# Optimization experiments

Hardware: AMD Instinct MI355X
Metric: run time of the kernel (lower is better)

The kernel has to match this reference:

```python
import jax, jax.numpy as jnp
import numpy as np

NU, NT, E, H, NL, NVOC, OUT, HID2 = 100000, 400000, 400000, 128, 3, 10000, 2, 64
EPS = 1e-5


def setup_inputs() -> dict:
    key = jax.random.key(0)
    ks = jax.random.split(key, 20)
    s = 1.0 / np.sqrt(H).astype(np.float32)
    inp = {
        "x_user": jax.random.randint(ks[0], (NU,), 0, NVOC),
        "x_txn": jax.random.randint(ks[1], (NT,), 0, NVOC),
        "ei0_src": jax.random.randint(ks[2], (E,), 0, NU),
        "ei0_dst": jax.random.randint(ks[3], (E,), 0, NT),
        "ei1_src": jax.random.randint(ks[4], (E,), 0, NT),
        "ei1_dst": jax.random.randint(ks[5], (E,), 0, NU),
        "emb_user": jax.random.normal(ks[6], (NVOC, H), jnp.float32),
        "emb_txn": jax.random.normal(ks[7], (NVOC, H), jnp.float32),
        "Wl": jax.random.normal(ks[8], (NL, 2, H, H), jnp.float32) * s,
        "bl": jax.random.normal(ks[9], (NL, 2, H), jnp.float32) * 0.01,
        "Wr": jax.random.normal(ks[10], (NL, 2, H, H), jnp.float32) * s,
        "bn_gamma": jax.random.uniform(ks[11], (NL, 2, H), jnp.float32, 0.5, 1.5),
        "bn_beta": jax.random.normal(ks[12], (NL, 2, H), jnp.float32) * 0.01,
        "bn_mean": jax.random.normal(ks[13], (NL, 2, H), jnp.float32) * 0.01,
        "bn_var": jax.random.uniform(ks[14], (NL, 2, H), jnp.float32, 0.5, 1.5),
        "W1": jax.random.normal(ks[15], (H, HID2), jnp.float32) * s,
        "b1": jax.random.normal(ks[16], (HID2,), jnp.float32) * 0.01,
        "W2": jax.random.normal(ks[17], (HID2, OUT), jnp.float32) * (1.0 / np.sqrt(HID2).astype(np.float32)),
        "b2": jax.random.normal(ks[18], (OUT,), jnp.float32) * 0.01,
    }
    return inp


def _seg_mean(src_feat, src_idx, dst_idx, num_dst):
    # gather per-edge src features, mean-reduce per dst node (SAGEConv aggr='mean')
    msg = src_feat[src_idx]                                        # [E, H]
    tot = jax.ops.segment_sum(msg, dst_idx, num_segments=num_dst)  # [Ndst, H]
    cnt = jax.ops.segment_sum(jnp.ones((dst_idx.shape[0], 1), src_feat.dtype),
                              dst_idx, num_segments=num_dst)
    return tot / jnp.maximum(cnt, 1.0)


def _bn_relu(x, g, b, m, v):
    return jax.nn.relu((x - m) * jax.lax.rsqrt(v + EPS) * g + b)


def reference(x_user, x_txn, ei0_src, ei0_dst, ei1_src, ei1_dst,
              emb_user, emb_txn, Wl, bl, Wr,
              bn_gamma, bn_beta, bn_mean, bn_var, W1, b1, W2, b2):
    h_u = emb_user[x_user]   # [NU, H]
    h_t = emb_txn[x_txn]     # [NT, H]
    for i in range(NL):
        # edge type 0: user -> transaction; edge type 1: transaction -> user
        agg_t = _seg_mean(h_u, ei0_src, ei0_dst, h_t.shape[0])
        agg_u = _seg_mean(h_t, ei1_src, ei1_dst, h_u.shape[0])
        new_t = agg_t @ Wl[i, 0] + bl[i, 0] + h_t @ Wr[i, 0]
        new_u = agg_u @ Wl[i, 1] + bl[i, 1] + h_u @ Wr[i, 1]
        h_u = _bn_relu(new_u, bn_gamma[i, 0], bn_beta[i, 0], bn_mean[i, 0], bn_var[i, 0])
        h_t = _bn_relu(new_t, bn_gamma[i, 1], bn_beta[i, 1], bn_mean[i, 1], bn_var[i, 1])
    h = jnp.concatenate([h_u, h_t], axis=0)            # [NU+NT, H]
    out = jax.nn.relu(h @ W1 + b1) @ W2 + b2           # [NU+NT, OUT]
    return out
```

## Files before the change

### kernel.cpp

```cpp
#include <hip/hip_runtime.h>


#define NUv   100000
#define NTv   400000
#define Ev    400000
#define Hv    128
#define NLv   3
#define HID2v 64
#define EPSv  1e-5f

typedef _Float16 h16;
typedef __attribute__((ext_vector_type(8))) _Float16 f16x8;
typedef __attribute__((ext_vector_type(4))) float    f32x4;

#define WS_NEED (280u * 1024u * 1024u)
__device__ __attribute__((aligned(256))) static unsigned char g_ws[WS_NEED];

__device__ __forceinline__ int imin(int a, int b) { return a < b ? a : b; }
__device__ __forceinline__ int swz(int n, int kbyte) {
  return n * 256 + (kbyte ^ ((n & 7) << 4));
}
__device__ __forceinline__ int swzB(int n, int kbyte) {
  return n * 512 + (kbyte ^ ((n & 7) << 4));
}

__global__ __launch_bounds__(256) void k_count(const int* __restrict__ d0,
                                               const int* __restrict__ d1,
                                               int* __restrict__ c0,
                                               int* __restrict__ c1, int e) {
  int t = blockIdx.x * 256 + threadIdx.x;
  if (t < e) {
    atomicAdd(c0 + d0[t], 1);
    atomicAdd(c1 + d1[t], 1);
  }
}

__global__ __launch_bounds__(256) void k_blocksum2(const int* __restrict__ c0,
                                                   int n0, int g0,
                                                   const int* __restrict__ c1,
                                                   int n1,
                                                   int* __restrict__ bs0,
                                                   int* __restrict__ bs1) {
  __shared__ int red[256];
  int second = blockIdx.x >= g0 ? 1 : 0;
  const int* cnt = second ? c1 : c0;
  int n = second ? n1 : n0;
  int* bs = second ? bs1 : bs0;
  int bid = blockIdx.x - (second ? g0 : 0);
  int base = bid * 2048 + threadIdx.x * 8;
  int s = 0;
#pragma unroll
  for (int j = 0; j < 8; j++) {
    int p = base + j;
    if (p < n) s += cnt[p];
  }
  red[threadIdx.x] = s;
  __syncthreads();
  for (int st = 128; st > 0; st >>= 1) {
    if (threadIdx.x < st) red[threadIdx.x] += red[threadIdx.x + st];
    __syncthreads();
  }
  if (threadIdx.x == 0) bs[bid] = red[0];
}

__global__ __launch_bounds__(256) void k_scansmall2(int* __restrict__ bs0, int g0,
                                                    int* __restrict__ bs1, int g1) {
  __shared__ int lds[256];
  int* bs = blockIdx.x ? bs1 : bs0;
  int g = blockIdx.x ? g1 : g0;
  int t = threadIdx.x;
  int v = (t < g) ? bs[t] : 0;
  lds[t] = v;
  __syncthreads();
  for (int st = 1; st < 256; st <<= 1) {
    int x = (t >= st) ? lds[t - st] : 0;
    __syncthreads();
    lds[t] += x;
    __syncthreads();
  }
  if (t < g) bs[t] = lds[t] - v;
}

__global__ __launch_bounds__(256) void k_scanfinal2(const int* __restrict__ c0,
                                                    int n0, int g0,
                                                    const int* __restrict__ bs0,
                                                    int* __restrict__ off0,
                                                    int* __restrict__ cur0,
                                                    const int* __restrict__ c1,
                                                    int n1,
                                                    const int* __restrict__ bs1,
                                                    int* __restrict__ off1,
                                                    int* __restrict__ cur1) {
  __shared__ int lds[256];
  int second = blockIdx.x >= g0 ? 1 : 0;
  const int* cnt = second ? c1 : c0;
  const int* bs = second ? bs1 : bs0;
  int* off = second ? off1 : off0;
  int* cur = second ? cur1 : cur0;
  int n = second ? n1 : n0;
  int bid = blockIdx.x - (second ? g0 : 0);
  int t = threadIdx.x;
  int base = bid * 2048 + t * 8;
  int v[8], pre[8];
  int tsum = 0;
#pragma unroll
  for (int j = 0; j < 8; j++) {
    int p = base + j;
    v[j] = (p < n) ? cnt[p] : 0;
    pre[j] = tsum;
    tsum += v[j];
  }
  lds[t] = tsum;
  __syncthreads();
  for (int st = 1; st < 256; st <<= 1) {
    int x = (t >= st) ? lds[t - st] : 0;
    __syncthreads();
    lds[t] += x;
    __syncthreads();
  }
  int texcl = lds[t] - tsum;
  int boff = bs[bid];
#pragma unroll
  for (int j = 0; j < 8; j++) {
    int p = base + j;
    if (p < n) {
      int o = boff + texcl + pre[j];
      off[p] = o;
      cur[p] = o;
      if (p == n - 1) off[n] = o + v[j];
    }
  }
}

__global__ __launch_bounds__(256) void k_fill(const int* __restrict__ s0,
                                              const int* __restrict__ d0,
                                              const int* __restrict__ s1,
                                              const int* __restrict__ d1,
                                              int* __restrict__ cur0,
                                              int* __restrict__ cur1,
                                              int* __restrict__ ss0,
                                              int* __restrict__ ss1, int e) {
  int t = blockIdx.x * 256 + threadIdx.x;
  if (t < e) {
    int p = atomicAdd(cur0 + d0[t], 1);
    ss0[p] = s0[t];
    int q = atomicAdd(cur1 + d1[t], 1);
    ss1[q] = s1[t];
  }
}

__global__ __launch_bounds__(256) void k_wtbn(const float* __restrict__ Wl,
                                              const float* __restrict__ Wr,
                                              const float* __restrict__ W1,
                                              const float* __restrict__ g,
                                              const float* __restrict__ b,
                                              const float* __restrict__ m,
                                              const float* __restrict__ v,
                                              h16* __restrict__ WlT,
                                              h16* __restrict__ WrT,
                                              h16* __restrict__ W1T,
                                              float* __restrict__ sc,
                                              float* __restrict__ sh) {
  int t = blockIdx.x * 256 + threadIdx.x;
  const int NW = NLv * 2 * Hv * Hv;
  const int NW1 = NW + HID2v * Hv;
  if (t < NW) {
    int mat = t / (Hv * Hv);
    int n = (t / Hv) % Hv;
    int k = t % Hv;
    WlT[t] = (h16)Wl[(size_t)mat * Hv * Hv + (size_t)k * Hv + n];
    WrT[t] = (h16)Wr[(size_t)mat * Hv * Hv + (size_t)k * Hv + n];
  } else if (t < NW1) {
    int u = t - NW;
    int n = u / Hv;
    int k = u % Hv;
    W1T[u] = (h16)W1[(size_t)k * HID2v + n];
  } else if (t < NW1 + NLv * 2 * Hv) {
    int u = t - NW1;
    float inv = rsqrtf(v[u] + EPSv);
    float s = g[u] * inv;
    sc[u] = s;
    sh[u] = b[u] - m[u] * s;
  }
}

__global__ __launch_bounds__(256) void k_embed(const int* __restrict__ xu,
                                               const int* __restrict__ xt,
                                               const float* __restrict__ eu,
                                               const float* __restrict__ et,
                                               h16* __restrict__ hu,
                                               h16* __restrict__ ht) {
  int t = blockIdx.x * 256 + threadIdx.x;
  int row = t >> 4;
  int c = (t & 15) * 8;
  if (row >= NUv + NTv) return;
  const float* src;
  h16* dst;
  if (row < NUv) {
    src = eu + (size_t)xu[row] * Hv;
    dst = hu + (size_t)row * Hv;
  } else {
    int r2 = row - NUv;
    src = et + (size_t)xt[r2] * Hv;
    dst = ht + (size_t)r2 * Hv;
  }
  float4 v0 = *(const float4*)(src + c);
  float4 v1 = *(const float4*)(src + c + 4);
  f16x8 o;
  o[0] = (h16)v0.x; o[1] = (h16)v0.y; o[2] = (h16)v0.z; o[3] = (h16)v0.w;
  o[4] = (h16)v1.x; o[5] = (h16)v1.y; o[6] = (h16)v1.z; o[7] = (h16)v1.w;
  *(f16x8*)(dst + c) = o;
}

__global__ __launch_bounds__(512, 4) void k_fused2(
    const h16* __restrict__ SRC0, const h16* __restrict__ DEN0,
    const int* __restrict__ offA, const int* __restrict__ ssA,
    const h16* __restrict__ BTl0, const h16* __restrict__ BTr0,
    const float* __restrict__ blp0, const float* __restrict__ scp0,
    const float* __restrict__ shp0, h16* __restrict__ C0, int M0,
    const h16* __restrict__ SRC1, const h16* __restrict__ DEN1,
    const int* __restrict__ offB, const int* __restrict__ ssB,
    const h16* __restrict__ BTl1, const h16* __restrict__ BTr1,
    const float* __restrict__ blp1, const float* __restrict__ scp1,
    const float* __restrict__ shp1, h16* __restrict__ C1, int M1) {
  __shared__ __align__(16) unsigned char sB[128 * 512];
  __shared__ __align__(16) unsigned char sA[64 * 256];

  int t = threadIdx.x;
  int l = t & 63, lm = l & 15, lk = l >> 4;
  int w = t >> 6, rg = w >> 1, cg = w & 1;

  int nT0 = (M0 + 63) / 64;
  int nT1 = (M1 + 63) / 64;
  int nTot = nT0 + nT1;
  int curDir = -1;

  for (int gidx = blockIdx.x; gidx < nTot; gidx += gridDim.x) {
    int dir = (gidx < nT0) ? 0 : 1;
    const h16* SRC = dir ? SRC1 : SRC0;
    const h16* DENSE = dir ? DEN1 : DEN0;
    const int* off = dir ? offB : offA;
    const int* ss = dir ? ssB : ssA;
    const float* blp = dir ? blp1 : blp0;
    const float* scp = dir ? scp1 : scp0;
    const float* shp = dir ? shp1 : shp0;
    h16* C = dir ? C1 : C0;
    int M = dir ? M1 : M0;
    int base = (dir ? gidx - nT0 : gidx) * 64;

    if (dir != curDir) {
      const h16* BTr = dir ? BTr1 : BTr0;
      const h16* BTl = dir ? BTl1 : BTl0;
      int n = t >> 2;
      int kb = (t & 3) * 64;
      const h16* sr = BTr + t * 32;
      f16x8 r0 = *(const f16x8*)(sr + 0);
      f16x8 r1 = *(const f16x8*)(sr + 8);
      f16x8 r2 = *(const f16x8*)(sr + 16);
      f16x8 r3 = *(const f16x8*)(sr + 24);
      const h16* sl = BTl + t * 32;
      f16x8 l0 = *(const f16x8*)(sl + 0);
      f16x8 l1 = *(const f16x8*)(sl + 8);
      f16x8 l2 = *(const f16x8*)(sl + 16);
      f16x8 l3 = *(const f16x8*)(sl + 24);
      *(f16x8*)(sB + swzB(n, kb + 0)) = r0;
      *(f16x8*)(sB + swzB(n, kb + 16)) = r1;
      *(f16x8*)(sB + swzB(n, kb + 32)) = r2;
      *(f16x8*)(sB + swzB(n, kb + 48)) = r3;
      *(f16x8*)(sB + swzB(n, 256 + kb + 0)) = l0;
      *(f16x8*)(sB + swzB(n, 256 + kb + 16)) = l1;
      *(f16x8*)(sB + swzB(n, 256 + kb + 32)) = l2;
      *(f16x8*)(sB + swzB(n, 256 + kb + 48)) = l3;
      __syncthreads();
      curDir = dir;
    }

    int ar = imin(base + rg * 16 + lm, M - 1);
    const h16* arow = DENSE + (size_t)ar * Hv;
    f16x8 ad0 = *(const f16x8*)(arow + 0 * 32 + lk * 8);
    f16x8 ad1 = *(const f16x8*)(arow + 1 * 32 + lk * 8);
    f16x8 ad2 = *(const f16x8*)(arow + 2 * 32 + lk * 8);
    f16x8 ad3 = *(const f16x8*)(arow + 3 * 32 + lk * 8);

    {
      int r = t >> 3;
      int cs = (t & 7) * 16;
      float facc[16];
#pragma unroll
      for (int j = 0; j < 16; j++) facc[j] = 0.f;
      int row = base + r;
      if (row < M) {
        int e0 = off[row], e1 = off[row + 1];
        for (int e = e0; e < e1; e += 2) {
          int i0 = ss[e];
          bool v1 = (e + 1) < e1;
          int i1 = v1 ? ss[e + 1] : i0;
          const f16x8* p0 = (const f16x8*)(SRC + (size_t)i0 * Hv + cs);
          const f16x8* p1 = (const f16x8*)(SRC + (size_t)i1 * Hv + cs);
          f16x8 x0 = p0[0], x1 = p0[1];
          f16x8 y0 = p1[0], y1 = p1[1];
          float m1 = v1 ? 1.f : 0.f;
#pragma unroll
          for (int j = 0; j < 8; j++) {
            facc[j] += (float)x0[j];
            facc[8 + j] += (float)x1[j];
            facc[j] = fmaf((float)y0[j], m1, facc[j]);
            facc[8 + j] = fmaf((float)y1[j], m1, facc[8 + j]);
          }
        }
        int deg = e1 - e0;
        float inv = 1.f / (float)(deg > 1 ? deg : 1);
#pragma unroll
        for (int j = 0; j < 16; j++) facc[j] *= inv;
      }
#pragma unroll
      for (int q = 0; q < 2; q++) {
        f16x8 ov;
#pragma unroll
        for (int j = 0; j < 8; j++) ov[j] = (h16)facc[q * 8 + j];
        *(f16x8*)(sA + swz(r, cs * 2 + q * 16)) = ov;
      }
    }
    __syncthreads();

    f32x4 acc[4];
#pragma unroll
    for (int j = 0; j < 4; j++) acc[j] = (f32x4){0.f, 0.f, 0.f, 0.f};
    {
      f16x8 ads[4] = {ad0, ad1, ad2, ad3};
#pragma unroll
      for (int s = 0; s < 4; s++) {
#pragma unroll
        for (int j = 0; j < 4; j++) {
          int n = (cg * 4 + j) * 16 + lm;
          f16x8 b = *(const f16x8*)(sB + swzB(n, s * 64 + lk * 16));
          acc[j] = __builtin_amdgcn_mfma_f32_16x16x32_f16(ads[s], b, acc[j], 0, 0, 0);
        }
      }
#pragma unroll
      for (int s = 0; s < 4; s++) {
        f16x8 a = *(const f16x8*)(sA + swz(rg * 16 + lm, s * 64 + lk * 16));
#pragma unroll
        for (int j = 0; j < 4; j++) {
          int n = (cg * 4 + j) * 16 + lm;
          f16x8 b = *(const f16x8*)(sB + swzB(n, 256 + s * 64 + lk * 16));
          acc[j] = __builtin_amdgcn_mfma_f32_16x16x32_f16(a, b, acc[j], 0, 0, 0);
        }
      }
    }

#pragma unroll
    for (int j = 0; j < 4; j++) {
      int col = (cg * 4 + j) * 16 + lm;
      float blv = blp[col], scv = scp[col], shv = shp[col];
#pragma unroll
      for (int r_ = 0; r_ < 4; r_++) {
        int row = base + rg * 16 + lk * 4 + r_;
        if (row < M) {
          float x = fmaf(acc[j][r_] + blv, scv, shv);
          C[(size_t)row * Hv + col] = (h16)fmaxf(x, 0.f);
        }
      }
    }
    __syncthreads();
  }
}

__global__ __launch_bounds__(512, 4) void k_mlp(const h16* __restrict__ HU,
                                                const h16* __restrict__ HT,
                                                const h16* __restrict__ W1T,
                                                const float* __restrict__ b1,
                                                const float* __restrict__ W2,
                                                const float* __restrict__ b2,
                                                float* __restrict__ out, int Mtot) {
  __shared__ float y[128][65];
  __shared__ __align__(16) unsigned char sW[64 * 256];
  int t = threadIdx.x;
  int w = t >> 6, l = t & 63;
  int lm = l & 15, lk = l >> 4;

  {
    const h16* src = W1T + t * 16;
    f16x8 w0 = *(const f16x8*)(src + 0);
    f16x8 w1 = *(const f16x8*)(src + 8);
    int n = (t * 16) >> 7;
    int kb = ((t * 16) & 127) * 2;
    *(f16x8*)(sW + swz(n, kb + 0)) = w0;
    *(f16x8*)(sW + swz(n, kb + 16)) = w1;
  }

  int rowBase = blockIdx.x * 128 + w * 16;
  int ar = imin(rowBase + lm, Mtot - 1);
  const h16* arow =
      (ar < NUv) ? (HU + (size_t)ar * Hv) : (HT + (size_t)(ar - NUv) * Hv);
  f16x8 a0 = *(const f16x8*)(arow + 0 * 32 + lk * 8);
  f16x8 a1 = *(const f16x8*)(arow + 1 * 32 + lk * 8);
  f16x8 a2 = *(const f16x8*)(arow + 2 * 32 + lk * 8);
  f16x8 a3 = *(const f16x8*)(arow + 3 * 32 + lk * 8);
  __syncthreads();

  f32x4 acc[4];
#pragma unroll
  for (int nf = 0; nf < 4; nf++) acc[nf] = (f32x4){0.f, 0.f, 0.f, 0.f};
  {
    f16x8 as[4] = {a0, a1, a2, a3};
#pragma unroll
    for (int s = 0; s < 4; s++) {
#pragma unroll
      for (int nf = 0; nf < 4; nf++) {
        f16x8 b = *(const f16x8*)(sW + swz(nf * 16 + lm, s * 64 + lk * 16));
        acc[nf] = __builtin_amdgcn_mfma_f32_16x16x32_f16(as[s], b, acc[nf], 0, 0, 0);
      }
    }
  }
#pragma unroll
  for (int nf = 0; nf < 4; nf++) {
    int col = nf * 16 + lm;
    float b1v = b1[col];
#pragma unroll
    for (int r = 0; r < 4; r++) {
      int rloc = w * 16 + lk * 4 + r;
      y[rloc][col] = fmaxf(acc[nf][r] + b1v, 0.f);
    }
  }
  __syncthreads();
  if (t < 256) {
    int rloc = t >> 1, o = t & 1;
    int row = blockIdx.x * 128 + rloc;
    if (row < Mtot) {
      float sum = b2[o];
#pragma unroll
      for (int k = 0; k < HID2v; k++) sum += y[rloc][k] * W2[k * 2 + o];
      out[(size_t)row * 2 + o] = sum;
    }
  }
}

extern "C" void kernel_launch(void* const* d_in, const int* in_sizes, int n_in,
                              void* d_out, int out_size, void* d_ws, size_t ws_size,
                              hipStream_t stream) {
  (void)in_sizes; (void)n_in; (void)out_size;

  const int* x_user  = (const int*)d_in[0];
  const int* x_txn   = (const int*)d_in[1];
  const int* ei0_src = (const int*)d_in[2];
  const int* ei0_dst = (const int*)d_in[3];
  const int* ei1_src = (const int*)d_in[4];
  const int* ei1_dst = (const int*)d_in[5];
  const float* emb_user = (const float*)d_in[6];
  const float* emb_txn  = (const float*)d_in[7];
  const float* Wl = (const float*)d_in[8];
  const float* bl = (const float*)d_in[9];
  const float* Wr = (const float*)d_in[10];
  const float* bn_g = (const float*)d_in[11];
  const float* bn_b = (const float*)d_in[12];
  const float* bn_m = (const float*)d_in[13];
  const float* bn_v = (const float*)d_in[14];
  const float* W1 = (const float*)d_in[15];
  const float* b1 = (const float*)d_in[16];
  const float* W2 = (const float*)d_in[17];
  const float* b2 = (const float*)d_in[18];
  float* out = (float*)d_out;

  char* wsb;
  if (ws_size >= (size_t)WS_NEED) {
    wsb = (char*)d_ws;
  } else {
    void* sym = nullptr;
    hipGetSymbolAddress(&sym, HIP_SYMBOL(g_ws));
    wsb = (char*)sym;
  }
  size_t o = 0;
  auto alloc = [&](size_t bytes) -> void* {
    o = (o + 255) & ~(size_t)255;
    void* p = wsb + o;
    o += bytes;
    return p;
  };
  h16* hu0  = (h16*)alloc((size_t)NUv * Hv * 2);
  h16* hu1  = (h16*)alloc((size_t)NUv * Hv * 2);
  h16* ht0  = (h16*)alloc((size_t)NTv * Hv * 2);
  h16* ht1  = (h16*)alloc((size_t)NTv * Hv * 2);
  h16* WlT  = (h16*)alloc((size_t)NLv * 2 * Hv * Hv * 2);
  h16* WrT  = (h16*)alloc((size_t)NLv * 2 * Hv * Hv * 2);
  h16* W1T  = (h16*)alloc((size_t)HID2v * Hv * 2);
  float* bnsc = (float*)alloc((size_t)NLv * 2 * Hv * 4);
  float* bnsh = (float*)alloc((size_t)NLv * 2 * Hv * 4);
  int* off0 = (int*)alloc((size_t)(NTv + 1) * 4);
  int* off1 = (int*)alloc((size_t)(NUv + 1) * 4);
  int* cur0 = (int*)alloc((size_t)NTv * 4);
  int* cur1 = (int*)alloc((size_t)NUv * 4);
  int* ss0  = (int*)alloc((size_t)Ev * 4);
  int* ss1  = (int*)alloc((size_t)Ev * 4);
  int* bs0  = (int*)alloc(256 * 4);
  int* bs1  = (int*)alloc(256 * 4);

  const int G_E    = (Ev + 255) / 256;
  const int G_BS0  = (NTv + 2047) / 2048;
  const int G_BS1  = (NUv + 2047) / 2048;
  const int G_EMB  = ((NUv + NTv) * 16 + 255) / 256;
  const int N_WTBN = NLv * 2 * Hv * Hv + HID2v * Hv + NLv * 2 * Hv;
  const int G_WTBN = (N_WTBN + 255) / 256;
  const int G_F    = 512;
  const int G_MLP  = (NUv + NTv + 127) / 128;

  hipMemsetAsync(cur0, 0, (size_t)NTv * 4, stream);
  hipMemsetAsync(cur1, 0, (size_t)NUv * 4, stream);
  k_count<<<G_E, 256, 0, stream>>>(ei0_dst, ei1_dst, cur0, cur1, Ev);
  k_blocksum2<<<G_BS0 + G_BS1, 256, 0, stream>>>(cur0, NTv, G_BS0, cur1, NUv,
                                                 bs0, bs1);
  k_scansmall2<<<2, 256, 0, stream>>>(bs0, G_BS0, bs1, G_BS1);
  k_scanfinal2<<<G_BS0 + G_BS1, 256, 0, stream>>>(cur0, NTv, G_BS0, bs0, off0,
                                                  cur0, cur1, NUv, bs1, off1,
                                                  cur1);
  k_fill<<<G_E, 256, 0, stream>>>(ei0_src, ei0_dst, ei1_src, ei1_dst,
                                  cur0, cur1, ss0, ss1, Ev);

  k_wtbn<<<G_WTBN, 256, 0, stream>>>(Wl, Wr, W1, bn_g, bn_b, bn_m, bn_v,
                                     WlT, WrT, W1T, bnsc, bnsh);

  k_embed<<<G_EMB, 256, 0, stream>>>(x_user, x_txn, emb_user, emb_txn, hu0, ht0);

  h16* hu_cur = hu0; h16* hu_nxt = hu1;
  h16* ht_cur = ht0; h16* ht_nxt = ht1;
  for (int i = 0; i < NLv; i++) {
    const h16* WlT0 = WlT + (size_t)(i * 2 + 0) * Hv * Hv;
    const h16* WlT1 = WlT + (size_t)(i * 2 + 1) * Hv * Hv;
    const h16* WrT0 = WrT + (size_t)(i * 2 + 0) * Hv * Hv;
    const h16* WrT1 = WrT + (size_t)(i * 2 + 1) * Hv * Hv;
    const float* bl0 = bl + (size_t)(i * 2 + 0) * Hv;
    const float* bl1 = bl + (size_t)(i * 2 + 1) * Hv;
    const float* sc0 = bnsc + (size_t)(i * 2 + 0) * Hv;
    const float* sh0 = bnsh + (size_t)(i * 2 + 0) * Hv;
    const float* sc1 = bnsc + (size_t)(i * 2 + 1) * Hv;
    const float* sh1 = bnsh + (size_t)(i * 2 + 1) * Hv;

    k_fused2<<<G_F, 512, 0, stream>>>(
        hu_cur, ht_cur, off0, ss0, WlT0, WrT0, bl0, sc1, sh1, ht_nxt, NTv,
        ht_cur, hu_cur, off1, ss1, WlT1, WrT1, bl1, sc0, sh0, hu_nxt, NUv);
    h16* tmp;
    tmp = ht_cur; ht_cur = ht_nxt; ht_nxt = tmp;
    tmp = hu_cur; hu_cur = hu_nxt; hu_nxt = tmp;
  }

  k_mlp<<<G_MLP, 512, 0, stream>>>(hu_cur, ht_cur, W1T, b1, W2, b2, out,
                                   NUv + NTv);
}
```

Measured before the change: 706.8 us.

## Restructure fused SAGE layer to per-wave 16-row tiles without LDS staging

The combined two-direction kernel becomes a single-direction kernel launched twice per layer. Each wave now owns a 16-row tile: it gathers neighbour features straight into MFMA A-operand registers, dropping the shared-memory A buffer and the per-tile block barriers. The bias is folded into the BN shift and the scale/shift values are hoisted out of the loop. In exchange it adds an extra launch per layer and higher register pressure from 32 float accumulators and 8 MFMA accumulators. Bounds checks are removed, so the code relies on M being a multiple of 16.

```diff
diff --git a/kernel.cpp b/kernel.cpp
--- a/kernel.cpp
+++ b/kernel.cpp
@@ -212,157 +212,128 @@
   *(f16x8*)(dst + c) = o;
 }
 
-__global__ __launch_bounds__(512, 4) void k_fused2(
-    const h16* __restrict__ SRC0, const h16* __restrict__ DEN0,
-    const int* __restrict__ offA, const int* __restrict__ ssA,
-    const h16* __restrict__ BTl0, const h16* __restrict__ BTr0,
-    const float* __restrict__ blp0, const float* __restrict__ scp0,
-    const float* __restrict__ shp0, h16* __restrict__ C0, int M0,
-    const h16* __restrict__ SRC1, const h16* __restrict__ DEN1,
-    const int* __restrict__ offB, const int* __restrict__ ssB,
-    const h16* __restrict__ BTl1, const h16* __restrict__ BTr1,
-    const float* __restrict__ blp1, const float* __restrict__ scp1,
-    const float* __restrict__ shp1, h16* __restrict__ C1, int M1) {
+__global__ __launch_bounds__(512, 4) void k_fused(const h16* __restrict__ SRC,
+                                                  const h16* __restrict__ DENSE,
+                                                  const int* __restrict__ off,
+                                                  const int* __restrict__ ss,
+                                                  const h16* __restrict__ BTl,
+                                                  const h16* __restrict__ BTr,
+                                                  const float* __restrict__ bl,
+                                                  const float* __restrict__ sc,
+                                                  const float* __restrict__ sh,
+                                                  h16* __restrict__ C, int M) {
   __shared__ __align__(16) unsigned char sB[128 * 512];
-  __shared__ __align__(16) unsigned char sA[64 * 256];
 
   int t = threadIdx.x;
   int l = t & 63, lm = l & 15, lk = l >> 4;
-  int w = t >> 6, rg = w >> 1, cg = w & 1;
-
-  int nT0 = (M0 + 63) / 64;
-  int nT1 = (M1 + 63) / 64;
-  int nTot = nT0 + nT1;
-  int curDir = -1;
-
-  for (int gidx = blockIdx.x; gidx < nTot; gidx += gridDim.x) {
-    int dir = (gidx < nT0) ? 0 : 1;
-    const h16* SRC = dir ? SRC1 : SRC0;
-    const h16* DENSE = dir ? DEN1 : DEN0;
-    const int* off = dir ? offB : offA;
-    const int* ss = dir ? ssB : ssA;
-    const float* blp = dir ? blp1 : blp0;
-    const float* scp = dir ? scp1 : scp0;
-    const float* shp = dir ? shp1 : shp0;
-    h16* C = dir ? C1 : C0;
-    int M = dir ? M1 : M0;
-    int base = (dir ? gidx - nT0 : gidx) * 64;
-
-    if (dir != curDir) {
-      const h16* BTr = dir ? BTr1 : BTr0;
-      const h16* BTl = dir ? BTl1 : BTl0;
-      int n = t >> 2;
-      int kb = (t & 3) * 64;
-      const h16* sr = BTr + t * 32;
-      f16x8 r0 = *(const f16x8*)(sr + 0);
-      f16x8 r1 = *(const f16x8*)(sr + 8);
-      f16x8 r2 = *(const f16x8*)(sr + 16);
-      f16x8 r3 = *(const f16x8*)(sr + 24);
-      const h16* sl = BTl + t * 32;
-      f16x8 l0 = *(const f16x8*)(sl + 0);
-      f16x8 l1 = *(const f16x8*)(sl + 8);
-      f16x8 l2 = *(const f16x8*)(sl + 16);
-      f16x8 l3 = *(const f16x8*)(sl + 24);
-      *(f16x8*)(sB + swzB(n, kb + 0)) = r0;
-      *(f16x8*)(sB + swzB(n, kb + 16)) = r1;
-      *(f16x8*)(sB + swzB(n, kb + 32)) = r2;
-      *(f16x8*)(sB + swzB(n, kb + 48)) = r3;
-      *(f16x8*)(sB + swzB(n, 256 + kb + 0)) = l0;
-      *(f16x8*)(sB + swzB(n, 256 + kb + 16)) = l1;
-      *(f16x8*)(sB + swzB(n, 256 + kb + 32)) = l2;
-      *(f16x8*)(sB + swzB(n, 256 + kb + 48)) = l3;
-      __syncthreads();
-      curDir = dir;
-    }
-
-    int ar = imin(base + rg * 16 + lm, M - 1);
-    const h16* arow = DENSE + (size_t)ar * Hv;
-    f16x8 ad0 = *(const f16x8*)(arow + 0 * 32 + lk * 8);
-    f16x8 ad1 = *(const f16x8*)(arow + 1 * 32 + lk * 8);
-    f16x8 ad2 = *(const f16x8*)(arow + 2 * 32 + lk * 8);
-    f16x8 ad3 = *(const f16x8*)(arow + 3 * 32 + lk * 8);
-
+  int w = t >> 6;
+
+  {
+    int n = t >> 2;
+    int kb = (t & 3) * 64;
+    const h16* sr = BTr + t * 32;
+    f16x8 r0 = *(const f16x8*)(sr + 0);
+    f16x8 r1 = *(const f16x8*)(sr + 8);
+    f16x8 r2 = *(const f16x8*)(sr + 16);
+    f16x8 r3 = *(const f16x8*)(sr + 24);
+    const h16* sl = BTl + t * 32;
+    f16x8 l0 = *(const f16x8*)(sl + 0);
+    f16x8 l1 = *(const f16x8*)(sl + 8);
+    f16x8 l2 = *(const f16x8*)(sl + 16);
+    f16x8 l3 = *(const f16x8*)(sl + 24);
+    *(f16x8*)(sB + swzB(n, kb + 0)) = r0;
+    *(f16x8*)(sB + swzB(n, kb + 16)) = r1;
+    *(f16x8*)(sB + swzB(n, kb + 32)) = r2;
+    *(f16x8*)(sB + swzB(n, kb + 48)) = r3;
+    *(f16x8*)(sB + swzB(n, 256 + kb + 0)) = l0;
+    *(f16x8*)(sB + swzB(n, 256 + kb + 16)) = l1;
+    *(f16x8*)(sB + swzB(n, 256 + kb + 32)) = l2;
+    *(f16x8*)(sB + swzB(n, 256 + kb + 48)) = l3;
+  }
+
+  float scv[8], shv[8];
+#pragma unroll
+  for (int j = 0; j < 8; j++) {
+    int col = j * 16 + lm;
+    float s = sc[col];
+    scv[j] = s;
+    shv[j] = fmaf(bl[col], s, sh[col]);
+  }
+  __syncthreads();
+
+  int nWT = M >> 4;
+  for (int wt = blockIdx.x * 8 + w; wt < nWT; wt += gridDim.x * 8) {
+    int base = wt << 4;
+    int rowA = base + lm;
+
+    const h16* arow = DENSE + (size_t)rowA * Hv + lk * 8;
+    f16x8 ad0 = *(const f16x8*)(arow);
+    f16x8 ad1 = *(const f16x8*)(arow + 32);
+    f16x8 ad2 = *(const f16x8*)(arow + 64);
+    f16x8 ad3 = *(const f16x8*)(arow + 96);
+
+    float facc[32];
+#pragma unroll
+    for (int j = 0; j < 32; j++) facc[j] = 0.f;
+    int e0 = off[rowA], e1 = off[rowA + 1];
+    for (int e = e0; e < e1; ++e) {
+      const h16* sp = SRC + (size_t)ss[e] * Hv + lk * 8;
+      f16x8 v0 = *(const f16x8*)(sp);
+      f16x8 v1 = *(const f16x8*)(sp + 32);
+      f16x8 v2 = *(const f16x8*)(sp + 64);
+      f16x8 v3 = *(const f16x8*)(sp + 96);
+#pragma unroll
+      for (int j = 0; j < 8; j++) {
+        facc[j] += (float)v0[j];
+        facc[8 + j] += (float)v1[j];
+        facc[16 + j] += (float)v2[j];
+        facc[24 + j] += (float)v3[j];
+      }
+    }
     {
-      int r = t >> 3;
-      int cs = (t & 7) * 16;
-      float facc[16];
-#pragma unroll
-      for (int j = 0; j < 16; j++) facc[j] = 0.f;
-      int row = base + r;
-      if (row < M) {
-        int e0 = off[row], e1 = off[row + 1];
-        for (int e = e0; e < e1; e += 2) {
-          int i0 = ss[e];
-          bool v1 = (e + 1) < e1;
-          int i1 = v1 ? ss[e + 1] : i0;
-          const f16x8* p0 = (const f16x8*)(SRC + (size_t)i0 * Hv + cs);
-          const f16x8* p1 = (const f16x8*)(SRC + (size_t)i1 * Hv + cs);
-          f16x8 x0 = p0[0], x1 = p0[1];
-          f16x8 y0 = p1[0], y1 = p1[1];
-          float m1 = v1 ? 1.f : 0.f;
-#pragma unroll
-          for (int j = 0; j < 8; j++) {
-            facc[j] += (float)x0[j];
-            facc[8 + j] += (float)x1[j];
-            facc[j] = fmaf((float)y0[j], m1, facc[j]);
-            facc[8 + j] = fmaf((float)y1[j], m1, facc[8 + j]);
-          }
-        }
-        int deg = e1 - e0;
-        float inv = 1.f / (float)(deg > 1 ? deg : 1);
-#pragma unroll
-        for (int j = 0; j < 16; j++) facc[j] *= inv;
-      }
-#pragma unroll
-      for (int q = 0; q < 2; q++) {
-        f16x8 ov;
-#pragma unroll
-        for (int j = 0; j < 8; j++) ov[j] = (h16)facc[q * 8 + j];
-        *(f16x8*)(sA + swz(r, cs * 2 + q * 16)) = ov;
-      }
-    }
-    __syncthreads();
-
-    f32x4 acc[4];
-#pragma unroll
-    for (int j = 0; j < 4; j++) acc[j] = (f32x4){0.f, 0.f, 0.f, 0.f};
+      int deg = e1 - e0;
+      float inv = 1.f / (float)(deg > 1 ? deg : 1);
+#pragma unroll
+      for (int j = 0; j < 32; j++) facc[j] *= inv;
+    }
+    f16x8 aA0, aA1, aA2, aA3;
+#pragma unroll
+    for (int j = 0; j < 8; j++) {
+      aA0[j] = (h16)facc[j];
+      aA1[j] = (h16)facc[8 + j];
+      aA2[j] = (h16)facc[16 + j];
+      aA3[j] = (h16)facc[24 + j];
+    }
+
+    f32x4 acc[8];
+#pragma unroll
+    for (int j = 0; j < 8; j++) acc[j] = (f32x4){0.f, 0.f, 0.f, 0.f};
     {
       f16x8 ads[4] = {ad0, ad1, ad2, ad3};
+      f16x8 aAs[4] = {aA0, aA1, aA2, aA3};
 #pragma unroll
       for (int s = 0; s < 4; s++) {
 #pragma unroll
-        for (int j = 0; j < 4; j++) {
-          int n = (cg * 4 + j) * 16 + lm;
-          f16x8 b = *(const f16x8*)(sB + swzB(n, s * 64 + lk * 16));
-          acc[j] = __builtin_amdgcn_mfma_f32_16x16x32_f16(ads[s], b, acc[j], 0, 0, 0);
+        for (int j = 0; j < 8; j++) {
+          int n = j * 16 + lm;
+          f16x8 br = *(const f16x8*)(sB + swzB(n, s * 64 + lk * 16));
+          acc[j] = __builtin_amdgcn_mfma_f32_16x16x32_f16(ads[s], br, acc[j], 0, 0, 0);
+          f16x8 bw = *(const f16x8*)(sB + swzB(n, 256 + s * 64 + lk * 16));
+          acc[j] = __builtin_amdgcn_mfma_f32_16x16x32_f16(aAs[s], bw, acc[j], 0, 0, 0);
         }
       }
-#pragma unroll
-      for (int s = 0; s < 4; s++) {
-        f16x8 a = *(const f16x8*)(sA + swz(rg * 16 + lm, s * 64 + lk * 16));
-#pragma unroll
-        for (int j = 0; j < 4; j++) {
-          int n = (cg * 4 + j) * 16 + lm;
-          f16x8 b = *(const f16x8*)(sB + swzB(n, 256 + s * 64 + lk * 16));
-          acc[j] = __builtin_amdgcn_mfma_f32_16x16x32_f16(a, b, acc[j], 0, 0, 0);
-        }
+    }
+
+#pragma unroll
+    for (int j = 0; j < 8; j++) {
+      int col = j * 16 + lm;
+#pragma unroll
+      for (int r_ = 0; r_ < 4; r_++) {
+        int row = base + lk * 4 + r_;
+        float x = fmaf(acc[j][r_], scv[j], shv[j]);
+        C[(size_t)row * Hv + col] = (h16)fmaxf(x, 0.f);
       }
     }
-
-#pragma unroll
-    for (int j = 0; j < 4; j++) {
-      int col = (cg * 4 + j) * 16 + lm;
-      float blv = blp[col], scv = scp[col], shv = shp[col];
-#pragma unroll
-      for (int r_ = 0; r_ < 4; r_++) {
-        int row = base + rg * 16 + lk * 4 + r_;
-        if (row < M) {
-          float x = fmaf(acc[j][r_] + blv, scv, shv);
-          C[(size_t)row * Hv + col] = (h16)fmaxf(x, 0.f);
-        }
-      }
-    }
-    __syncthreads();
   }
 }
 
@@ -535,9 +506,10 @@
     const float* sc1 = bnsc + (size_t)(i * 2 + 1) * Hv;
     const float* sh1 = bnsh + (size_t)(i * 2 + 1) * Hv;
 
-    k_fused2<<<G_F, 512, 0, stream>>>(
-        hu_cur, ht_cur, off0, ss0, WlT0, WrT0, bl0, sc1, sh1, ht_nxt, NTv,
-        ht_cur, hu_cur, off1, ss1, WlT1, WrT1, bl1, sc0, sh0, hu_nxt, NUv);
+    k_fused<<<G_F, 512, 0, stream>>>(hu_cur, ht_cur, off0, ss0, WlT0, WrT0,
+                                     bl0, sc1, sh1, ht_nxt, NTv);
+    k_fused<<<G_F, 512, 0, stream>>>(ht_cur, hu_cur, off1, ss1, WlT1, WrT1,
+                                     bl1, sc0, sh0, hu_nxt, NUv);
     h16* tmp;
     tmp = ht_cur; ht_cur = ht_nxt; ht_nxt = tmp;
     tmp = hu_cur; hu_cur = hu_nxt; hu_nxt = tmp;
```

Result: slower. 2.002 ms (+183.2%).

## Sort destination rows by in-degree and split fused layer into per-direction launches

Applied to the files above, without the earlier changes.

Adds a degree-histogram counting sort that builds a permutation of destination rows grouped by in-degree. The fused aggregate+GEMM kernel then processes rows in that order, so rows within a tile have similar edge counts and per-thread gather loops are more balanced. The single two-direction kernel is split into two launches, each loading its weights once up front, and bias is folded into the BN shift. The cost is three extra preprocessing kernels, an indirection through perm on dense loads and output stores, scattered row writes, and a launch boundary between the two directions.

```diff
diff --git a/kernel.cpp b/kernel.cpp
--- a/kernel.cpp
+++ b/kernel.cpp
@@ -146,6 +146,79 @@
     ss0[p] = s0[t];
     int q = atomicAdd(cur1 + d1[t], 1);
     ss1[q] = s1[t];
+  }
+}
+
+__global__ __launch_bounds__(256) void k_deghist2(const int* __restrict__ off0,
+                                                  int n0, int g0,
+                                                  const int* __restrict__ off1,
+                                                  int n1,
+                                                  int* __restrict__ h0,
+                                                  int* __restrict__ h1) {
+  __shared__ int lh[32];
+  int t = threadIdx.x;
+  if (t < 32) lh[t] = 0;
+  __syncthreads();
+  int second = blockIdx.x >= g0 ? 1 : 0;
+  const int* off = second ? off1 : off0;
+  int n = second ? n1 : n0;
+  int* h = second ? h1 : h0;
+  int r = (blockIdx.x - (second ? g0 : 0)) * 256 + t;
+  if (r < n) {
+    int d = off[r + 1] - off[r];
+    if (d > 31) d = 31;
+    atomicAdd(&lh[d], 1);
+  }
+  __syncthreads();
+  if (t < 32 && lh[t]) atomicAdd(&h[t], lh[t]);
+}
+
+__global__ __launch_bounds__(64) void k_degscan2(int* __restrict__ h0,
+                                                 int* __restrict__ h1) {
+  int* h = blockIdx.x ? h1 : h0;
+  if (threadIdx.x == 0) {
+    int s = 0;
+    for (int i = 0; i < 32; i++) {
+      int v = h[i];
+      h[i] = s;
+      s += v;
+    }
+  }
+}
+
+__global__ __launch_bounds__(256) void k_degscatter2(const int* __restrict__ off0,
+                                                     int n0, int g0,
+                                                     const int* __restrict__ off1,
+                                                     int n1,
+                                                     int* __restrict__ cur0,
+                                                     int* __restrict__ cur1,
+                                                     int* __restrict__ p0,
+                                                     int* __restrict__ p1) {
+  __shared__ int lh[32], lstart[32];
+  int t = threadIdx.x;
+  if (t < 32) lh[t] = 0;
+  __syncthreads();
+  int second = blockIdx.x >= g0 ? 1 : 0;
+  const int* off = second ? off1 : off0;
+  int n = second ? n1 : n0;
+  int* cur = second ? cur1 : cur0;
+  int* perm = second ? p1 : p0;
+  int r = (blockIdx.x - (second ? g0 : 0)) * 256 + t;
+  int bin = 0;
+  if (r < n) {
+    int d = off[r + 1] - off[r];
+    bin = d > 31 ? 31 : d;
+    atomicAdd(&lh[bin], 1);
+  }
+  __syncthreads();
+  if (t < 32) {
+    if (lh[t]) lstart[t] = atomicAdd(&cur[t], lh[t]);
+    lh[t] = 0;
+  }
+  __syncthreads();
+  if (r < n) {
+    int rank = atomicAdd(&lh[bin], 1);
+    perm[lstart[bin] + rank] = r;
   }
 }
 
@@ -212,71 +285,66 @@
   *(f16x8*)(dst + c) = o;
 }
 
-__global__ __launch_bounds__(512, 4) void k_fused2(
-    const h16* __restrict__ SRC0, const h16* __restrict__ DEN0,
-    const int* __restrict__ offA, const int* __restrict__ ssA,
-    const h16* __restrict__ BTl0, const h16* __restrict__ BTr0,
-    const float* __restrict__ blp0, const float* __restrict__ scp0,
-    const float* __restrict__ shp0, h16* __restrict__ C0, int M0,
-    const h16* __restrict__ SRC1, const h16* __restrict__ DEN1,
-    const int* __restrict__ offB, const int* __restrict__ ssB,
-    const h16* __restrict__ BTl1, const h16* __restrict__ BTr1,
-    const float* __restrict__ blp1, const float* __restrict__ scp1,
-    const float* __restrict__ shp1, h16* __restrict__ C1, int M1) {
+__global__ __launch_bounds__(512, 4) void k_fused(const h16* __restrict__ SRC,
+                                                  const h16* __restrict__ DENSE,
+                                                  const int* __restrict__ off,
+                                                  const int* __restrict__ ss,
+                                                  const int* __restrict__ perm,
+                                                  const h16* __restrict__ BTl,
+                                                  const h16* __restrict__ BTr,
+                                                  const float* __restrict__ bl,
+                                                  const float* __restrict__ sc,
+                                                  const float* __restrict__ sh,
+                                                  h16* __restrict__ C, int M) {
   __shared__ __align__(16) unsigned char sB[128 * 512];
   __shared__ __align__(16) unsigned char sA[64 * 256];
 
   int t = threadIdx.x;
-  int l = t & 63, lm = l & 15, lk = l >> 4;
-  int w = t >> 6, rg = w >> 1, cg = w & 1;
-
-  int nT0 = (M0 + 63) / 64;
-  int nT1 = (M1 + 63) / 64;
-  int nTot = nT0 + nT1;
-  int curDir = -1;
-
-  for (int gidx = blockIdx.x; gidx < nTot; gidx += gridDim.x) {
-    int dir = (gidx < nT0) ? 0 : 1;
-    const h16* SRC = dir ? SRC1 : SRC0;
-    const h16* DENSE = dir ? DEN1 : DEN0;
-    const int* off = dir ? offB : offA;
-    const int* ss = dir ? ssB : ssA;
-    const float* blp = dir ? blp1 : blp0;
-    const float* scp = dir ? scp1 : scp0;
-    const float* shp = dir ? shp1 : shp0;
-    h16* C = dir ? C1 : C0;
-    int M = dir ? M1 : M0;
-    int base = (dir ? gidx - nT0 : gidx) * 64;
-
-    if (dir != curDir) {
-      const h16* BTr = dir ? BTr1 : BTr0;
-      const h16* BTl = dir ? BTl1 : BTl0;
-      int n = t >> 2;
-      int kb = (t & 3) * 64;
-      const h16* sr = BTr + t * 32;
-      f16x8 r0 = *(const f16x8*)(sr + 0);
-      f16x8 r1 = *(const f16x8*)(sr + 8);
-      f16x8 r2 = *(const f16x8*)(sr + 16);
-      f16x8 r3 = *(const f16x8*)(sr + 24);
-      const h16* sl = BTl + t * 32;
-      f16x8 l0 = *(const f16x8*)(sl + 0);
-      f16x8 l1 = *(const f16x8*)(sl + 8);
-      f16x8 l2 = *(const f16x8*)(sl + 16);
-      f16x8 l3 = *(const f16x8*)(sl + 24);
-      *(f16x8*)(sB + swzB(n, kb + 0)) = r0;
-      *(f16x8*)(sB + swzB(n, kb + 16)) = r1;
-      *(f16x8*)(sB + swzB(n, kb + 32)) = r2;
-      *(f16x8*)(sB + swzB(n, kb + 48)) = r3;
-      *(f16x8*)(sB + swzB(n, 256 + kb + 0)) = l0;
-      *(f16x8*)(sB + swzB(n, 256 + kb + 16)) = l1;
-      *(f16x8*)(sB + swzB(n, 256 + kb + 32)) = l2;
-      *(f16x8*)(sB + swzB(n, 256 + kb + 48)) = l3;
-      __syncthreads();
-      curDir = dir;
-    }
-
-    int ar = imin(base + rg * 16 + lm, M - 1);
-    const h16* arow = DENSE + (size_t)ar * Hv;
+  int l = t & 63;
+  int lm = l & 15, lk = l >> 4;
+  int w = t >> 6;
+  int rg = w >> 1, cg = w & 1;
+
+  {
+    int n = t >> 2;
+    int kb = (t & 3) * 64;
+    const h16* sr = BTr + t * 32;
+    f16x8 r0 = *(const f16x8*)(sr + 0);
+    f16x8 r1 = *(const f16x8*)(sr + 8);
+    f16x8 r2 = *(const f16x8*)(sr + 16);
+    f16x8 r3 = *(const f16x8*)(sr + 24);
+    const h16* sl = BTl + t * 32;
+    f16x8 l0 = *(const f16x8*)(sl + 0);
+    f16x8 l1 = *(const f16x8*)(sl + 8);
+    f16x8 l2 = *(const f16x8*)(sl + 16);
+    f16x8 l3 = *(const f16x8*)(sl + 24);
+    *(f16x8*)(sB + swzB(n, kb + 0)) = r0;
+    *(f16x8*)(sB + swzB(n, kb + 16)) = r1;
+    *(f16x8*)(sB + swzB(n, kb + 32)) = r2;
+    *(f16x8*)(sB + swzB(n, kb + 48)) = r3;
+    *(f16x8*)(sB + swzB(n, 256 + kb + 0)) = l0;
+    *(f16x8*)(sB + swzB(n, 256 + kb + 16)) = l1;
+    *(f16x8*)(sB + swzB(n, 256 + kb + 32)) = l2;
+    *(f16x8*)(sB + swzB(n, 256 + kb + 48)) = l3;
+  }
+
+  float scv[4], shv[4];
+#pragma unroll
+  for (int j = 0; j < 4; j++) {
+    int col = (cg * 4 + j) * 16 + lm;
+    float s = sc[col];
+    scv[j] = s;
+    shv[j] = fmaf(bl[col], s, sh[col]);
+  }
+  __syncthreads();
+
+  int nTiles = (M + 63) / 64;
+  for (int tile = blockIdx.x; tile < nTiles; tile += gridDim.x) {
+    int base = tile * 64;
+
+    int posD = imin(base + rg * 16 + lm, M - 1);
+    int prowD = perm[posD];
+    const h16* arow = DENSE + (size_t)prowD * Hv;
     f16x8 ad0 = *(const f16x8*)(arow + 0 * 32 + lk * 8);
     f16x8 ad1 = *(const f16x8*)(arow + 1 * 32 + lk * 8);
     f16x8 ad2 = *(const f16x8*)(arow + 2 * 32 + lk * 8);
@@ -288,9 +356,10 @@
       float facc[16];
 #pragma unroll
       for (int j = 0; j < 16; j++) facc[j] = 0.f;
-      int row = base + r;
-      if (row < M) {
-        int e0 = off[row], e1 = off[row + 1];
+      int pos = base + r;
+      if (pos < M) {
+        int prow = perm[pos];
+        int e0 = off[prow], e1 = off[prow + 1];
         for (int e = e0; e < e1; e += 2) {
           int i0 = ss[e];
           bool v1 = (e + 1) < e1;
@@ -349,16 +418,20 @@
       }
     }
 
+    int prowS[4];
+#pragma unroll
+    for (int r_ = 0; r_ < 4; r_++) {
+      int pos = base + rg * 16 + lk * 4 + r_;
+      prowS[r_] = (pos < M) ? perm[pos] : -1;
+    }
 #pragma unroll
     for (int j = 0; j < 4; j++) {
       int col = (cg * 4 + j) * 16 + lm;
-      float blv = blp[col], scv = scp[col], shv = shp[col];
 #pragma unroll
       for (int r_ = 0; r_ < 4; r_++) {
-        int row = base + rg * 16 + lk * 4 + r_;
-        if (row < M) {
-          float x = fmaf(acc[j][r_] + blv, scv, shv);
-          C[(size_t)row * Hv + col] = (h16)fmaxf(x, 0.f);
+        if (prowS[r_] >= 0) {
+          float x = fmaf(acc[j][r_], scv[j], shv[j]);
+          C[(size_t)prowS[r_] * Hv + col] = (h16)fmaxf(x, 0.f);
         }
       }
     }
@@ -494,10 +567,16 @@
   int* ss1  = (int*)alloc((size_t)Ev * 4);
   int* bs0  = (int*)alloc(256 * 4);
   int* bs1  = (int*)alloc(256 * 4);
+  int* perm0 = (int*)alloc((size_t)NTv * 4);
+  int* perm1 = (int*)alloc((size_t)NUv * 4);
+  int* hist0 = (int*)alloc(32 * 4);
+  int* hist1 = (int*)alloc(32 * 4);
 
   const int G_E    = (Ev + 255) / 256;
   const int G_BS0  = (NTv + 2047) / 2048;
   const int G_BS1  = (NUv + 2047) / 2048;
+  const int G_R0   = (NTv + 255) / 256;
+  const int G_R1   = (NUv + 255) / 256;
   const int G_EMB  = ((NUv + NTv) * 16 + 255) / 256;
   const int N_WTBN = NLv * 2 * Hv * Hv + HID2v * Hv + NLv * 2 * Hv;
   const int G_WTBN = (N_WTBN + 255) / 256;
@@ -506,6 +585,8 @@
 
   hipMemsetAsync(cur0, 0, (size_t)NTv * 4, stream);
   hipMemsetAsync(cur1, 0, (size_t)NUv * 4, stream);
+  hipMemsetAsync(hist0, 0, 32 * 4, stream);
+  hipMemsetAsync(hist1, 0, 32 * 4, stream);
   k_count<<<G_E, 256, 0, stream>>>(ei0_dst, ei1_dst, cur0, cur1, Ev);
   k_blocksum2<<<G_BS0 + G_BS1, 256, 0, stream>>>(cur0, NTv, G_BS0, cur1, NUv,
                                                  bs0, bs1);
@@ -515,6 +596,12 @@
                                                   cur1);
   k_fill<<<G_E, 256, 0, stream>>>(ei0_src, ei0_dst, ei1_src, ei1_dst,
                                   cur0, cur1, ss0, ss1, Ev);
+
+  k_deghist2<<<G_R0 + G_R1, 256, 0, stream>>>(off0, NTv, G_R0, off1, NUv,
+                                              hist0, hist1);
+  k_degscan2<<<2, 64, 0, stream>>>(hist0, hist1);
+  k_degscatter2<<<G_R0 + G_R1, 256, 0, stream>>>(off0, NTv, G_R0, off1, NUv,
+                                                 hist0, hist1, perm0, perm1);
 
   k_wtbn<<<G_WTBN, 256, 0, stream>>>(Wl, Wr, W1, bn_g, bn_b, bn_m, bn_v,
                                      WlT, WrT, W1T, bnsc, bnsh);
@@ -535,9 +622,10 @@
     const float* sc1 = bnsc + (size_t)(i * 2 + 1) * Hv;
     const float* sh1 = bnsh + (size_t)(i * 2 + 1) * Hv;
 
-    k_fused2<<<G_F, 512, 0, stream>>>(
-        hu_cur, ht_cur, off0, ss0, WlT0, WrT0, bl0, sc1, sh1, ht_nxt, NTv,
-        ht_cur, hu_cur, off1, ss1, WlT1, WrT1, bl1, sc0, sh0, hu_nxt, NUv);
+    k_fused<<<G_F, 512, 0, stream>>>(hu_cur, ht_cur, off0, ss0, perm0,
+                                     WlT0, WrT0, bl0, sc1, sh1, ht_nxt, NTv);
+    k_fused<<<G_F, 512, 0, stream>>>(ht_cur, hu_cur, off1, ss1, perm1,
+                                     WlT1, WrT1, bl1, sc0, sh0, hu_nxt, NUv);
     h16* tmp;
     tmp = ht_cur; ht_cur = ht_nxt; ht_nxt = tmp;
     tmp = hu_cur; hu_cur = hu_nxt; hu_nxt = tmp;
```

Measured after the change: 654.0 us. -7.5%, faster.
